# Kernel optimization log

Measured on AMD Instinct MI355X. Metric: run time of the kernel, lower is better.

## Reference

```python
import jax, jax.numpy as jnp
import numpy as np

B, S, D, H, FF = 2, 4096, 1024, 16, 4096
HD = D // H


def _layernorm(x, g, b, eps=1e-5):
    mu = jnp.mean(x, axis=-1, keepdims=True)
    var = jnp.var(x, axis=-1, keepdims=True)
    return (x - mu) * jax.lax.rsqrt(var + eps) * g + b


def setup_inputs() -> dict:
    key = jax.random.key(0)
    ks = jax.random.split(key, 20)
    sd = 1.0 / np.sqrt(D)
    sf = 1.0 / np.sqrt(FF)
    inp = {
        "x": jax.random.normal(ks[0], (B, S, D), jnp.float32),
        # attention projections, stored as [in, out]
        "wq": jax.random.normal(ks[1], (D, D), jnp.float32) * sd,
        "bq": jnp.zeros((D,), jnp.float32),
        "wk": jax.random.normal(ks[2], (D, D), jnp.float32) * sd,
        "bk": jnp.zeros((D,), jnp.float32),
        "wv": jax.random.normal(ks[3], (D, D), jnp.float32) * sd,
        "bv": jnp.zeros((D,), jnp.float32),
        "wo": jax.random.normal(ks[4], (D, D), jnp.float32) * sd,
        "bo": jnp.zeros((D,), jnp.float32),
        # block norm1 (pre-attention)
        "ln1_g": jnp.ones((D,), jnp.float32),
        "ln1_b": jnp.zeros((D,), jnp.float32),
        # FFN internal norm
        "lnf_g": jnp.ones((D,), jnp.float32),
        "lnf_b": jnp.zeros((D,), jnp.float32),
        # gated FFN
        "w1": jax.random.normal(ks[5], (D, FF), jnp.float32) * sd,
        "b1": jnp.zeros((FF,), jnp.float32),
        "wg": jax.random.normal(ks[6], (D, FF), jnp.float32) * sd,
        "bg": jnp.zeros((FF,), jnp.float32),
        "w2": jax.random.normal(ks[7], (FF, D), jnp.float32) * sf,
        "b2": jnp.zeros((D,), jnp.float32),
    }
    return inp


def reference(x, wq, bq, wk, bk, wv, bv, wo, bo, ln1_g, ln1_b,
              lnf_g, lnf_b, w1, b1, wg, bg, w2, b2):
    # pre-norm attention
    residual = x
    h = _layernorm(x, ln1_g, ln1_b)
    q = (h @ wq + bq).reshape(B, S, H, HD).transpose(0, 2, 1, 3)  # [B,H,S,hd]
    k = (h @ wk + bk).reshape(B, S, H, HD).transpose(0, 2, 1, 3)
    v = (h @ wv + bv).reshape(B, S, H, HD).transpose(0, 2, 1, 3)
    scores = jnp.einsum("bhqd,bhkd->bhqk", q, k) / np.sqrt(HD)
    attn = jax.nn.softmax(scores, axis=-1)  # [B,H,S,S] materialized as in torch src
    ctx = jnp.einsum("bhqk,bhkd->bhqd", attn, v)
    ctx = ctx.transpose(0, 2, 1, 3).reshape(B, S, D)
    attn_out = ctx @ wo + bo
    x = residual + attn_out  # dropout = 0 (eval)

    # gated FFN with internal pre-norm and residual
    res2 = x
    h2 = _layernorm(x, lnf_g, lnf_b)
    gate = jax.nn.sigmoid(h2 @ wg + bg)
    up = jax.nn.gelu(h2 @ w1 + b1, approximate=False)
    out = (up * gate) @ w2 + b2
    return out + res2
```

## Files before the change

kernel.cpp:

```cpp
#include <hip/hip_runtime.h>
#include <hip/hip_bf16.h>

#define BB 2
#define SS 4096
#define DD 1024
#define HH 16
#define HD 64
#define FF 4096
#define MM (BB*SS)

typedef __hip_bfloat16 bf16;
typedef __attribute__((ext_vector_type(8))) __bf16 v8bf;
typedef __attribute__((ext_vector_type(4))) float f32x4;
typedef __attribute__((ext_vector_type(16))) float f32x16;
typedef __attribute__((ext_vector_type(8))) unsigned short u16v8;

__device__ __forceinline__ f32x4 mfma16(v8bf a, v8bf b, f32x4 c) {
  return __builtin_amdgcn_mfma_f32_16x16x32_bf16(a, b, c, 0, 0, 0);
}
__device__ __forceinline__ f32x16 mfma32(v8bf a, v8bf b, f32x16 c) {
  return __builtin_amdgcn_mfma_f32_32x32x16_bf16(a, b, c, 0, 0, 0);
}
__device__ __forceinline__ void gload16(const void* g, void* l) {
  __builtin_amdgcn_global_load_lds((const __attribute__((address_space(1))) void*)g,
                                   (__attribute__((address_space(3))) void*)l, 16, 0, 0);
}
__device__ __forceinline__ unsigned cvtpk_bf16(float lo, float hi) {
  unsigned r;
  asm("v_cvt_pk_bf16_f32 %0, %1, %2" : "=v"(r) : "v"(lo), "v"(hi));
  return r;
}
__device__ __forceinline__ void xcd_swz(int& bx, int& by) {
  const int nwg = gridDim.x * gridDim.y;
  int o = blockIdx.y * gridDim.x + blockIdx.x;
  o = (o & 7) * (nwg >> 3) + (o >> 3);
  bx = o % gridDim.x;
  by = o / gridDim.x;
}

__global__ void k_tcvt(const float* __restrict__ W, bf16* __restrict__ Wt, int K, int N,
                       float scale)
{
  __shared__ float tile[32][33];
  const int n0 = blockIdx.x * 32, k0 = blockIdx.y * 32;
  const int tx = threadIdx.x, ty = threadIdx.y;
#pragma unroll
  for (int i = 0; i < 32; i += 8)
    tile[ty + i][tx] = W[(long)(k0 + ty + i) * N + n0 + tx];
  __syncthreads();
#pragma unroll
  for (int i = 0; i < 32; i += 8)
    Wt[(long)(n0 + ty + i) * K + k0 + tx] = __float2bfloat16(tile[tx][ty + i] * scale);
}

__global__ __launch_bounds__(256)
void k_vtrans(const bf16* __restrict__ V, bf16* __restrict__ Vt)
{
  __shared__ bf16 tile[64][72];
  const int s0 = blockIdx.x * 64;
  const int h  = blockIdx.y;
  const int b  = blockIdx.z;
  const int t  = threadIdx.x;
  const int r = t >> 3, c8 = t & 7;
#pragma unroll
  for (int it = 0; it < 2; ++it) {
    const int sr = it * 32 + r;
    const u16v8 v = *(const u16v8*)(V + (long)(b * SS + s0 + sr) * DD + h * 64 + c8 * 8);
#pragma unroll
    for (int e = 0; e < 8; ++e)
      ((unsigned short*)&tile[sr][0])[c8 * 8 + e] = v[e];
  }
  __syncthreads();
#pragma unroll
  for (int it = 0; it < 2; ++it) {
    const int d = it * 32 + r;
    union { unsigned short s[8]; u16v8 v; } o;
#pragma unroll
    for (int e = 0; e < 8; ++e)
      o.s[e] = ((const unsigned short*)tile)[(c8 * 8 + e) * 72 + d];
    *(u16v8*)(Vt + ((long)(b * HH + h) * HD + d) * (long)SS + s0 + c8 * 8) = o.v;
  }
}

__global__ __launch_bounds__(256)
void k_layernorm(const float* __restrict__ x, const float* __restrict__ g,
                 const float* __restrict__ b, bf16* __restrict__ out)
{
  const int row = blockIdx.x;
  const float4 v = ((const float4*)(x + (long)row * DD))[threadIdx.x];
  float s  = v.x + v.y + v.z + v.w;
  float s2 = v.x*v.x + v.y*v.y + v.z*v.z + v.w*v.w;
#pragma unroll
  for (int off = 1; off < 64; off <<= 1) {
    s  += __shfl_xor(s,  off);
    s2 += __shfl_xor(s2, off);
  }
  __shared__ float red[8];
  if ((threadIdx.x & 63) == 0) {
    red[threadIdx.x >> 6]       = s;
    red[(threadIdx.x >> 6) + 4] = s2;
  }
  __syncthreads();
  s  = red[0] + red[1] + red[2] + red[3];
  s2 = red[4] + red[5] + red[6] + red[7];
  const float mu = s * (1.f / DD);
  const float rs = rsqrtf(s2 * (1.f / DD) - mu * mu + 1e-5f);
  const float4 gv = ((const float4*)g)[threadIdx.x];
  const float4 bv = ((const float4*)b)[threadIdx.x];
  bf16* op = out + (long)row * DD + threadIdx.x * 4;
  op[0] = __float2bfloat16((v.x - mu) * rs * gv.x + bv.x);
  op[1] = __float2bfloat16((v.y - mu) * rs * gv.y + bv.y);
  op[2] = __float2bfloat16((v.z - mu) * rs * gv.z + bv.z);
  op[3] = __float2bfloat16((v.w - mu) * rs * gv.w + bv.w);
}

template<int EPI, int SWZ>
__global__ __launch_bounds__(256, 2)
void k_gemm(const bf16* __restrict__ A, const bf16* __restrict__ Bt,
            const float* __restrict__ bias, const float* __restrict__ res,
            void* __restrict__ Cout, int M, int N, int K, float scale)
{
  __shared__ __align__(16) bf16 As[128 * 32];
  __shared__ __align__(16) bf16 Bs[128 * 32];
  int bx = blockIdx.x, by = blockIdx.y;
  if (SWZ) xcd_swz(bx, by);
  const int t = threadIdx.x;
  const int lane = t & 63, w = t >> 6;
  const int wr = w >> 1, wc = w & 1;
  const int fr = lane & 15, fq = lane >> 4;
  const long m0 = (long)by * 128, n0 = (long)bx * 128;

  f32x4 acc[4][4] = {};

  const bf16* Ag0 = A  + (m0 + (t >> 2)) * K + (t & 3) * 8;
  const bf16* Ag1 = Ag0 + 64L * K;
  const bf16* Bg0 = Bt + (n0 + (t >> 2)) * K + (t & 3) * 8;
  const bf16* Bg1 = Bg0 + 64L * K;

  for (int kk = 0; kk < K; kk += 32) {
    gload16(Ag0 + kk, As + t * 8);
    gload16(Ag1 + kk, As + 2048 + t * 8);
    gload16(Bg0 + kk, Bs + t * 8);
    gload16(Bg1 + kk, Bs + 2048 + t * 8);
    __syncthreads();
    v8bf af[4], bfr[4];
#pragma unroll
    for (int mt = 0; mt < 4; ++mt)
      af[mt] = *(const v8bf*)&As[(wr*64 + mt*16 + fr) * 32 + fq*8];
#pragma unroll
    for (int nt = 0; nt < 4; ++nt)
      bfr[nt] = *(const v8bf*)&Bs[(wc*64 + nt*16 + fr) * 32 + fq*8];
#pragma unroll
    for (int mt = 0; mt < 4; ++mt)
#pragma unroll
      for (int nt = 0; nt < 4; ++nt)
        acc[mt][nt] = mfma16(af[mt], bfr[nt], acc[mt][nt]);
    __syncthreads();
  }

#pragma unroll
  for (int nt = 0; nt < 4; ++nt) {
    const long col = n0 + wc*64 + nt*16 + fr;
    const float bv = bias[col];
#pragma unroll
    for (int mt = 0; mt < 4; ++mt) {
#pragma unroll
      for (int j = 0; j < 4; ++j) {
        const long row = m0 + wr*64 + mt*16 + fq*4 + j;
        float v = (acc[mt][nt][j] + bv) * scale;
        if (EPI == 0) ((bf16*)Cout)[row * N + col] = __float2bfloat16(v);
        else          ((float*)Cout)[row * N + col] = v + res[row * N + col];
      }
    }
  }
}

__global__ __launch_bounds__(256, 2)
void k_ffn_dual(const bf16* __restrict__ A, const bf16* __restrict__ BgT,
                const bf16* __restrict__ BuT, const float* __restrict__ bgb,
                const float* __restrict__ bub, bf16* __restrict__ Out)
{
  __shared__ __align__(16) bf16 As[128 * 32];
  __shared__ __align__(16) bf16 Gs[64 * 32];
  __shared__ __align__(16) bf16 Us[64 * 32];
  const int t = threadIdx.x;
  const int lane = t & 63, w = t >> 6;
  const int wr = w >> 1, wc = w & 1;
  const int fr = lane & 15, fq = lane >> 4;
  const long m0 = (long)blockIdx.y * 128, n0 = (long)blockIdx.x * 64;
  const int K = DD;

  f32x4 ag[4][2] = {}, au[4][2] = {};

  const bf16* Ag0 = A   + (m0 + (t >> 2)) * K + (t & 3) * 8;
  const bf16* Ag1 = Ag0 + 64L * K;
  const bf16* Gg  = BgT + (n0 + (t >> 2)) * K + (t & 3) * 8;
  const bf16* Ug  = BuT + (n0 + (t >> 2)) * K + (t & 3) * 8;

  for (int kk = 0; kk < K; kk += 32) {
    gload16(Ag0 + kk, As + t * 8);
    gload16(Ag1 + kk, As + 2048 + t * 8);
    gload16(Gg + kk, Gs + t * 8);
    gload16(Ug + kk, Us + t * 8);
    __syncthreads();
    v8bf af[4], gf[2], uf[2];
#pragma unroll
    for (int mt = 0; mt < 4; ++mt)
      af[mt] = *(const v8bf*)&As[(wr*64 + mt*16 + fr) * 32 + fq*8];
#pragma unroll
    for (int nt = 0; nt < 2; ++nt) {
      gf[nt] = *(const v8bf*)&Gs[(wc*32 + nt*16 + fr) * 32 + fq*8];
      uf[nt] = *(const v8bf*)&Us[(wc*32 + nt*16 + fr) * 32 + fq*8];
    }
#pragma unroll
    for (int mt = 0; mt < 4; ++mt)
#pragma unroll
      for (int nt = 0; nt < 2; ++nt) {
        ag[mt][nt] = mfma16(af[mt], gf[nt], ag[mt][nt]);
        au[mt][nt] = mfma16(af[mt], uf[nt], au[mt][nt]);
      }
    __syncthreads();
  }

#pragma unroll
  for (int nt = 0; nt < 2; ++nt) {
    const long col = n0 + wc*32 + nt*16 + fr;
    const float gb = bgb[col], ub = bub[col];
#pragma unroll
    for (int mt = 0; mt < 4; ++mt) {
#pragma unroll
      for (int j = 0; j < 4; ++j) {
        const long row = m0 + wr*64 + mt*16 + fq*4 + j;
        const float g = ag[mt][nt][j] + gb;
        const float u = au[mt][nt][j] + ub;
        const float sg = 1.f / (1.f + __expf(-g));
        const float gl = 0.5f * u * (1.f + erff(u * 0.70710678118f));
        Out[row * FF + col] = __float2bfloat16(sg * gl);
      }
    }
  }
}

__global__ __launch_bounds__(256, 2)
void k_attn(const bf16* __restrict__ Qb, const bf16* __restrict__ Kb,
            const bf16* __restrict__ Vt, bf16* __restrict__ ctx)
{
  __shared__ __align__(16) bf16 Ksh[2][4096];
  __shared__ __align__(16) bf16 Vsh[2][4096];
  const int t = threadIdx.x;
  const int lane = t & 63, w = t >> 6;
  const int q5 = lane & 31, hi = lane >> 5;

  int o = blockIdx.x + 32 * (blockIdx.y + 16 * blockIdx.z);
  o = (o & 7) * 128 + (o >> 3);
  const int q0 = (o & 31) * 128;
  const int h = (o >> 5) & 15, b = o >> 9;

  const long qk_base = ((long)b * SS) * DD + h * HD;
  const long vt_base = ((long)(b * HH + h)) * ((long)HD * SS);

  const int r0 = t >> 3;
  const int cswz = ((t & 7) * 16) ^ ((r0 & 7) << 4);
  const bf16* kg = Kb + qk_base + (long)r0 * DD + (cswz >> 1);
  const bf16* vg = Vt + vt_base + (long)r0 * SS + (cswz >> 1);

  v8bf qf[4];
  {
    const bf16* qp = Qb + qk_base + (long)(q0 + w * 32 + q5) * DD + hi * 8;
#pragma unroll
    for (int c = 0; c < 4; ++c) qf[c] = *(const v8bf*)(qp + c * 16);
  }

  int kcol[4];
#pragma unroll
  for (int c = 0; c < 4; ++c)
    kcol[c] = ((c * 32 + hi * 16) ^ ((q5 & 7) << 4)) >> 1;

  float m_ = -1e30f, l_ = 0.f;
  f32x16 o0 = {}, o1 = {};

#define STAGE(bufidx, kv0_) do {                                  \
    const bf16* kp_ = kg + (long)(kv0_) * DD;                     \
    gload16(kp_,            &Ksh[bufidx][t * 8]);                 \
    gload16(kp_ + 32L * DD, &Ksh[bufidx][2048 + t * 8]);          \
    const bf16* vp_ = vg + (kv0_);                                \
    gload16(vp_,            &Vsh[bufidx][t * 8]);                 \
    gload16(vp_ + 32L * SS, &Vsh[bufidx][2048 + t * 8]);          \
  } while (0)

  STAGE(0, 0);
  __syncthreads();

  for (int tt = 0; tt < SS / 64; ++tt) {
    const int cur = tt & 1;
    if (tt + 1 < SS / 64) STAGE(cur ^ 1, (tt + 1) * 64);

    f32x16 s0 = {}, s1 = {};
#pragma unroll
    for (int c = 0; c < 4; ++c) {
      const v8bf k0 = *(const v8bf*)&Ksh[cur][q5 * 64 + kcol[c]];
      const v8bf k1 = *(const v8bf*)&Ksh[cur][(32 + q5) * 64 + kcol[c]];
      s0 = mfma32(k0, qf[c], s0);
      s1 = mfma32(k1, qf[c], s1);
    }

    float pm = s0[0];
#pragma unroll
    for (int r = 1; r < 16; ++r) pm = fmaxf(pm, s0[r]);
#pragma unroll
    for (int r = 0; r < 16; ++r) pm = fmaxf(pm, s1[r]);
    pm = fmaxf(pm, __shfl_xor(pm, 32));
    const float mn = fmaxf(m_, pm);
    const float al = __builtin_amdgcn_exp2f(m_ - mn);
    m_ = mn;
    float rs = 0.f;
#pragma unroll
    for (int r = 0; r < 16; ++r) { s0[r] = __builtin_amdgcn_exp2f(s0[r] - mn); rs += s0[r]; }
#pragma unroll
    for (int r = 0; r < 16; ++r) { s1[r] = __builtin_amdgcn_exp2f(s1[r] - mn); rs += s1[r]; }
    rs += __shfl_xor(rs, 32);
    l_ = l_ * al + rs;
#pragma unroll
    for (int r = 0; r < 16; ++r) { o0[r] *= al; o1[r] *= al; }

    v8bf pb[4];
#pragma unroll
    for (int c = 0; c < 4; ++c) {
      const int base = (c & 1) * 8;
      unsigned wa0, wa1, wb0, wb1;
      if (c < 2) {
        wa0 = cvtpk_bf16(s0[base + 0], s0[base + 1]);
        wa1 = cvtpk_bf16(s0[base + 2], s0[base + 3]);
        wb0 = cvtpk_bf16(s0[base + 4], s0[base + 5]);
        wb1 = cvtpk_bf16(s0[base + 6], s0[base + 7]);
      } else {
        wa0 = cvtpk_bf16(s1[base + 0], s1[base + 1]);
        wa1 = cvtpk_bf16(s1[base + 2], s1[base + 3]);
        wb0 = cvtpk_bf16(s1[base + 4], s1[base + 5]);
        wb1 = cvtpk_bf16(s1[base + 6], s1[base + 7]);
      }
      asm("v_permlane32_swap_b32 %0, %1" : "+v"(wa0), "+v"(wb0));
      asm("v_permlane32_swap_b32 %0, %1" : "+v"(wa1), "+v"(wb1));
      union { unsigned u[4]; v8bf v; } cvt;
      cvt.u[0] = wa0; cvt.u[1] = wa1; cvt.u[2] = wb0; cvt.u[3] = wb1;
      pb[c] = cvt.v;
    }

#pragma unroll
    for (int c = 0; c < 4; ++c) {
      const v8bf v0f = *(const v8bf*)&Vsh[cur][q5 * 64 + kcol[c]];
      const v8bf v1f = *(const v8bf*)&Vsh[cur][(32 + q5) * 64 + kcol[c]];
      o0 = mfma32(v0f, pb[c], o0);
      o1 = mfma32(v1f, pb[c], o1);
    }
    __syncthreads();
  }
#undef STAGE

  const float inv = 1.f / l_;
  bf16* Osh = &Ksh[0][0];
  const int qrow = w * 32 + q5;
  const int oswz = (qrow & 7) << 4;
#pragma unroll
  for (int r = 0; r < 16; ++r) {
    const int d0 = (r & 3) + 8 * (r >> 2) + 4 * hi;
    Osh[((qrow * 128 + d0 * 2) ^ oswz) >> 1]        = __float2bfloat16(o0[r] * inv);
    Osh[((qrow * 128 + (32 + d0) * 2) ^ oswz) >> 1] = __float2bfloat16(o1[r] * inv);
  }
  __syncthreads();
  {
    const int q = t >> 1, half = t & 1;
    const int qs = (q & 7) << 4;
    bf16* cp = ctx + qk_base + (long)(q0 + q) * DD + half * 32;
#pragma unroll
    for (int s = 0; s < 4; ++s) {
      const int byte = (q * 128 + half * 64 + s * 16) ^ qs;
      *(u16v8*)(cp + s * 8) = *(const u16v8*)&Osh[byte >> 1];
    }
  }
}

extern "C" void kernel_launch(void* const* d_in, const int* in_sizes, int n_in,
                              void* d_out, int out_size, void* d_ws, size_t ws_size,
                              hipStream_t stream)
{
  const float* x    = (const float*)d_in[0];
  const float* wq   = (const float*)d_in[1];
  const float* bq   = (const float*)d_in[2];
  const float* wk   = (const float*)d_in[3];
  const float* bk   = (const float*)d_in[4];
  const float* wv   = (const float*)d_in[5];
  const float* bv   = (const float*)d_in[6];
  const float* wo   = (const float*)d_in[7];
  const float* bo   = (const float*)d_in[8];
  const float* ln1g = (const float*)d_in[9];
  const float* ln1b = (const float*)d_in[10];
  const float* lnfg = (const float*)d_in[11];
  const float* lnfb = (const float*)d_in[12];
  const float* w1   = (const float*)d_in[13];
  const float* b1   = (const float*)d_in[14];
  const float* wg   = (const float*)d_in[15];
  const float* bg   = (const float*)d_in[16];
  const float* w2   = (const float*)d_in[17];
  const float* b2   = (const float*)d_in[18];

  char* ws = (char*)d_ws;
  const size_t MB = 1u << 20;
  bf16*  WqT  = (bf16*)(ws + 0 * MB);
  bf16*  WkT  = (bf16*)(ws + 2 * MB);
  bf16*  WvT  = (bf16*)(ws + 4 * MB);
  bf16*  WoT  = (bf16*)(ws + 6 * MB);
  bf16*  W1T  = (bf16*)(ws + 8 * MB);
  bf16*  WgT  = (bf16*)(ws + 16 * MB);
  bf16*  W2T  = (bf16*)(ws + 24 * MB);
  float* x1   = (float*)(ws + 32 * MB);
  bf16*  hbuf = (bf16*)(ws + 64 * MB);
  bf16*  Qb   = (bf16*)(ws + 80 * MB);
  bf16*  Kb   = (bf16*)(ws + 96 * MB);
  bf16*  Vb   = (bf16*)(ws + 112 * MB);
  bf16*  Vtb  = (bf16*)(ws + 128 * MB);
  bf16*  ctxb = hbuf;
  bf16*  prod = (bf16*)(ws + 80 * MB);

  const float qscale = 0.1803368801111204f;

  dim3 tb(32, 8);
  k_tcvt<<<dim3(32, 32), tb, 0, stream>>>(wq, WqT, 1024, 1024, 1.f);
  k_tcvt<<<dim3(32, 32), tb, 0, stream>>>(wk, WkT, 1024, 1024, 1.f);
  k_tcvt<<<dim3(32, 32), tb, 0, stream>>>(wv, WvT, 1024, 1024, 1.f);
  k_tcvt<<<dim3(32, 32), tb, 0, stream>>>(wo, WoT, 1024, 1024, 1.f);
  k_tcvt<<<dim3(128, 32), tb, 0, stream>>>(w1, W1T, 1024, 4096, 1.f);
  k_tcvt<<<dim3(128, 32), tb, 0, stream>>>(wg, WgT, 1024, 4096, 1.f);
  k_tcvt<<<dim3(32, 128), tb, 0, stream>>>(w2, W2T, 4096, 1024, 1.f);

  k_layernorm<<<MM, 256, 0, stream>>>(x, ln1g, ln1b, hbuf);

  dim3 g1(1024 / 128, MM / 128);
  k_gemm<0,1><<<g1, 256, 0, stream>>>(hbuf, WqT, bq, nullptr, Qb, MM, 1024, 1024, qscale);
  k_gemm<0,1><<<g1, 256, 0, stream>>>(hbuf, WkT, bk, nullptr, Kb, MM, 1024, 1024, 1.f);
  k_gemm<0,1><<<g1, 256, 0, stream>>>(hbuf, WvT, bv, nullptr, Vb, MM, 1024, 1024, 1.f);
  k_vtrans<<<dim3(SS / 64, HH, BB), 256, 0, stream>>>(Vb, Vtb);

  k_attn<<<dim3(SS / 128, HH, BB), 256, 0, stream>>>(Qb, Kb, Vtb, ctxb);

  k_gemm<1,1><<<g1, 256, 0, stream>>>(ctxb, WoT, bo, x, x1, MM, 1024, 1024, 1.f);

  k_layernorm<<<MM, 256, 0, stream>>>(x1, lnfg, lnfb, hbuf);

  k_ffn_dual<<<dim3(FF / 64, MM / 128), 256, 0, stream>>>(hbuf, WgT, W1T, bg, b1, prod);

  k_gemm<1,0><<<g1, 256, 0, stream>>>(prod, W2T, b2, x1, (float*)d_out, MM, 1024, 4096, 1.f);
}
```

Measured before the change: 621.3 us.

## Fuse QKV GEMMs, approximate GELU/sigmoid, add lazy softmax rescaling, drop swizzle

Concatenates Wq/Wk/Wv into one transposed weight, with the Q scale folded into the weights, and runs a single 3072-wide GEMM whose epilogue selects the bias per segment. The attention and V-transpose kernels read directly from the fused QKV buffer. The FFN epilogue replaces erf-GELU with a tanh-style exp approximation and uses hardware rcp for the sigmoid. Attention skips the online-softmax rescale when the running max grows by at most 8, and the XCD swizzle is disabled for every GEMM. These changes aim to cut launch overhead, redundant A-tile loads, and transcendental cost, at the price of some accuracy and possibly worse L2 locality.

After: 619.7 us. No clear change (-0.3%).

```diff
diff --git a/kernel.cpp b/kernel.cpp
--- a/kernel.cpp
+++ b/kernel.cpp
@@ -8,6 +8,7 @@
 #define HD 64
 #define FF 4096
 #define MM (BB*SS)
+#define QKVW 3072
 
 typedef __hip_bfloat16 bf16;
 typedef __attribute__((ext_vector_type(8))) __bf16 v8bf;
@@ -30,16 +31,14 @@
   asm("v_cvt_pk_bf16_f32 %0, %1, %2" : "=v"(r) : "v"(lo), "v"(hi));
   return r;
 }
-__device__ __forceinline__ void xcd_swz(int& bx, int& by) {
-  const int nwg = gridDim.x * gridDim.y;
-  int o = blockIdx.y * gridDim.x + blockIdx.x;
-  o = (o & 7) * (nwg >> 3) + (o >> 3);
-  bx = o % gridDim.x;
-  by = o / gridDim.x;
+__device__ __forceinline__ float fastrcp(float x) {
+  float r;
+  asm("v_rcp_f32 %0, %1" : "=v"(r) : "v"(x));
+  return r;
 }
 
 __global__ void k_tcvt(const float* __restrict__ W, bf16* __restrict__ Wt, int K, int N,
-                       float scale)
+                       long rowoff, float scale)
 {
   __shared__ float tile[32][33];
   const int n0 = blockIdx.x * 32, k0 = blockIdx.y * 32;
@@ -50,11 +49,11 @@
   __syncthreads();
 #pragma unroll
   for (int i = 0; i < 32; i += 8)
-    Wt[(long)(n0 + ty + i) * K + k0 + tx] = __float2bfloat16(tile[tx][ty + i] * scale);
+    Wt[(rowoff + n0 + ty + i) * K + k0 + tx] = __float2bfloat16(tile[tx][ty + i] * scale);
 }
 
 __global__ __launch_bounds__(256)
-void k_vtrans(const bf16* __restrict__ V, bf16* __restrict__ Vt)
+void k_vtrans(const bf16* __restrict__ qkv, bf16* __restrict__ Vt)
 {
   __shared__ bf16 tile[64][72];
   const int s0 = blockIdx.x * 64;
@@ -65,7 +64,8 @@
 #pragma unroll
   for (int it = 0; it < 2; ++it) {
     const int sr = it * 32 + r;
-    const u16v8 v = *(const u16v8*)(V + (long)(b * SS + s0 + sr) * DD + h * 64 + c8 * 8);
+    const u16v8 v =
+        *(const u16v8*)(qkv + (long)(b * SS + s0 + sr) * QKVW + 2048 + h * 64 + c8 * 8);
 #pragma unroll
     for (int e = 0; e < 8; ++e)
       ((unsigned short*)&tile[sr][0])[c8 * 8 + e] = v[e];
@@ -117,13 +117,20 @@
 template<int EPI, int SWZ>
 __global__ __launch_bounds__(256, 2)
 void k_gemm(const bf16* __restrict__ A, const bf16* __restrict__ Bt,
-            const float* __restrict__ bias, const float* __restrict__ res,
+            const float* __restrict__ bias, const float* __restrict__ bias2,
+            const float* __restrict__ bias3, const float* __restrict__ res,
             void* __restrict__ Cout, int M, int N, int K, float scale)
 {
   __shared__ __align__(16) bf16 As[128 * 32];
   __shared__ __align__(16) bf16 Bs[128 * 32];
   int bx = blockIdx.x, by = blockIdx.y;
-  if (SWZ) xcd_swz(bx, by);
+  if (SWZ) {
+    const int nwg = gridDim.x * gridDim.y;
+    int o = by * gridDim.x + bx;
+    o = (o & 7) * (nwg >> 3) + (o >> 3);
+    bx = o % gridDim.x;
+    by = o / gridDim.x;
+  }
   const int t = threadIdx.x;
   const int lane = t & 63, w = t >> 6;
   const int wr = w >> 1, wc = w & 1;
@@ -161,14 +168,21 @@
 #pragma unroll
   for (int nt = 0; nt < 4; ++nt) {
     const long col = n0 + wc*64 + nt*16 + fr;
-    const float bv = bias[col];
+    float bv;
+    if (EPI == 2) {
+      const int seg = (int)(col >> 10);
+      bv = (seg == 0) ? bias[col & 1023] * scale
+                      : ((seg == 1) ? bias2 : bias3)[col & 1023];
+    } else {
+      bv = bias[col];
+    }
 #pragma unroll
     for (int mt = 0; mt < 4; ++mt) {
 #pragma unroll
       for (int j = 0; j < 4; ++j) {
         const long row = m0 + wr*64 + mt*16 + fq*4 + j;
-        float v = (acc[mt][nt][j] + bv) * scale;
-        if (EPI == 0) ((bf16*)Cout)[row * N + col] = __float2bfloat16(v);
+        const float v = acc[mt][nt][j] + bv;
+        if (EPI == 2) ((bf16*)Cout)[row * N + col] = __float2bfloat16(v);
         else          ((float*)Cout)[row * N + col] = v + res[row * N + col];
       }
     }
@@ -233,8 +247,11 @@
         const long row = m0 + wr*64 + mt*16 + fq*4 + j;
         const float g = ag[mt][nt][j] + gb;
         const float u = au[mt][nt][j] + ub;
-        const float sg = 1.f / (1.f + __expf(-g));
-        const float gl = 0.5f * u * (1.f + erff(u * 0.70710678118f));
+        const float eg = __builtin_amdgcn_exp2f(1.44269504f * g);
+        const float sg = eg * fastrcp(1.f + eg);
+        const float u3 = u * u * u;
+        const float E = __builtin_amdgcn_exp2f(fmaf(0.1029453f, u3, 2.3021858f * u));
+        const float gl = u * E * fastrcp(1.f + E);
         Out[row * FF + col] = __float2bfloat16(sg * gl);
       }
     }
@@ -242,8 +259,8 @@
 }
 
 __global__ __launch_bounds__(256, 2)
-void k_attn(const bf16* __restrict__ Qb, const bf16* __restrict__ Kb,
-            const bf16* __restrict__ Vt, bf16* __restrict__ ctx)
+void k_attn(const bf16* __restrict__ qkv, const bf16* __restrict__ Vt,
+            bf16* __restrict__ ctx)
 {
   __shared__ __align__(16) bf16 Ksh[2][4096];
   __shared__ __align__(16) bf16 Vsh[2][4096];
@@ -256,17 +273,18 @@
   const int q0 = (o & 31) * 128;
   const int h = (o >> 5) & 15, b = o >> 9;
 
-  const long qk_base = ((long)b * SS) * DD + h * HD;
-  const long vt_base = ((long)(b * HH + h)) * ((long)HD * SS);
+  const long qkv_row0 = (long)b * SS * QKVW + h * HD;
+  const long ctx_base = (long)b * SS * DD + h * HD;
+  const long vt_base  = ((long)(b * HH + h)) * ((long)HD * SS);
 
   const int r0 = t >> 3;
   const int cswz = ((t & 7) * 16) ^ ((r0 & 7) << 4);
-  const bf16* kg = Kb + qk_base + (long)r0 * DD + (cswz >> 1);
+  const bf16* kg = qkv + qkv_row0 + 1024 + (long)r0 * QKVW + (cswz >> 1);
   const bf16* vg = Vt + vt_base + (long)r0 * SS + (cswz >> 1);
 
   v8bf qf[4];
   {
-    const bf16* qp = Qb + qk_base + (long)(q0 + w * 32 + q5) * DD + hi * 8;
+    const bf16* qp = qkv + qkv_row0 + (long)(q0 + w * 32 + q5) * QKVW + hi * 8;
 #pragma unroll
     for (int c = 0; c < 4; ++c) qf[c] = *(const v8bf*)(qp + c * 16);
   }
@@ -279,13 +297,13 @@
   float m_ = -1e30f, l_ = 0.f;
   f32x16 o0 = {}, o1 = {};
 
-#define STAGE(bufidx, kv0_) do {                                  \
-    const bf16* kp_ = kg + (long)(kv0_) * DD;                     \
-    gload16(kp_,            &Ksh[bufidx][t * 8]);                 \
-    gload16(kp_ + 32L * DD, &Ksh[bufidx][2048 + t * 8]);          \
-    const bf16* vp_ = vg + (kv0_);                                \
-    gload16(vp_,            &Vsh[bufidx][t * 8]);                 \
-    gload16(vp_ + 32L * SS, &Vsh[bufidx][2048 + t * 8]);          \
+#define STAGE(bufidx, kv0_) do {                                    \
+    const bf16* kp_ = kg + (long)(kv0_) * QKVW;                     \
+    gload16(kp_,              &Ksh[bufidx][t * 8]);                 \
+    gload16(kp_ + 32L * QKVW, &Ksh[bufidx][2048 + t * 8]);          \
+    const bf16* vp_ = vg + (kv0_);                                  \
+    gload16(vp_,            &Vsh[bufidx][t * 8]);                   \
+    gload16(vp_ + 32L * SS, &Vsh[bufidx][2048 + t * 8]);            \
   } while (0)
 
   STAGE(0, 0);
@@ -310,18 +328,28 @@
 #pragma unroll
     for (int r = 0; r < 16; ++r) pm = fmaxf(pm, s1[r]);
     pm = fmaxf(pm, __shfl_xor(pm, 32));
-    const float mn = fmaxf(m_, pm);
-    const float al = __builtin_amdgcn_exp2f(m_ - mn);
-    m_ = mn;
+
     float rs = 0.f;
-#pragma unroll
-    for (int r = 0; r < 16; ++r) { s0[r] = __builtin_amdgcn_exp2f(s0[r] - mn); rs += s0[r]; }
-#pragma unroll
-    for (int r = 0; r < 16; ++r) { s1[r] = __builtin_amdgcn_exp2f(s1[r] - mn); rs += s1[r]; }
-    rs += __shfl_xor(rs, 32);
-    l_ = l_ * al + rs;
-#pragma unroll
-    for (int r = 0; r < 16; ++r) { o0[r] *= al; o1[r] *= al; }
+    if (__all(pm - m_ <= 8.f)) {
+#pragma unroll
+      for (int r = 0; r < 16; ++r) { s0[r] = __builtin_amdgcn_exp2f(s0[r] - m_); rs += s0[r]; }
+#pragma unroll
+      for (int r = 0; r < 16; ++r) { s1[r] = __builtin_amdgcn_exp2f(s1[r] - m_); rs += s1[r]; }
+      rs += __shfl_xor(rs, 32);
+      l_ += rs;
+    } else {
+      const float mn = fmaxf(m_, pm);
+      const float al = __builtin_amdgcn_exp2f(m_ - mn);
+      m_ = mn;
+#pragma unroll
+      for (int r = 0; r < 16; ++r) { s0[r] = __builtin_amdgcn_exp2f(s0[r] - mn); rs += s0[r]; }
+#pragma unroll
+      for (int r = 0; r < 16; ++r) { s1[r] = __builtin_amdgcn_exp2f(s1[r] - mn); rs += s1[r]; }
+      rs += __shfl_xor(rs, 32);
+      l_ = l_ * al + rs;
+#pragma unroll
+      for (int r = 0; r < 16; ++r) { o0[r] *= al; o1[r] *= al; }
+    }
 
     v8bf pb[4];
 #pragma unroll
@@ -371,7 +399,7 @@
   {
     const int q = t >> 1, half = t & 1;
     const int qs = (q & 7) << 4;
-    bf16* cp = ctx + qk_base + (long)(q0 + q) * DD + half * 32;
+    bf16* cp = ctx + ctx_base + (long)(q0 + q) * DD + half * 32;
 #pragma unroll
     for (int s = 0; s < 4; ++s) {
       const int byte = (q * 128 + half * 64 + s * 16) ^ qs;
@@ -406,48 +434,44 @@
 
   char* ws = (char*)d_ws;
   const size_t MB = 1u << 20;
-  bf16*  WqT  = (bf16*)(ws + 0 * MB);
-  bf16*  WkT  = (bf16*)(ws + 2 * MB);
-  bf16*  WvT  = (bf16*)(ws + 4 * MB);
-  bf16*  WoT  = (bf16*)(ws + 6 * MB);
-  bf16*  W1T  = (bf16*)(ws + 8 * MB);
-  bf16*  WgT  = (bf16*)(ws + 16 * MB);
-  bf16*  W2T  = (bf16*)(ws + 24 * MB);
-  float* x1   = (float*)(ws + 32 * MB);
-  bf16*  hbuf = (bf16*)(ws + 64 * MB);
-  bf16*  Qb   = (bf16*)(ws + 80 * MB);
-  bf16*  Kb   = (bf16*)(ws + 96 * MB);
-  bf16*  Vb   = (bf16*)(ws + 112 * MB);
-  bf16*  Vtb  = (bf16*)(ws + 128 * MB);
-  bf16*  ctxb = hbuf;
-  bf16*  prod = (bf16*)(ws + 80 * MB);
+  bf16*  WqkvT = (bf16*)(ws + 0 * MB);
+  bf16*  WoT   = (bf16*)(ws + 6 * MB);
+  bf16*  W1T   = (bf16*)(ws + 8 * MB);
+  bf16*  WgT   = (bf16*)(ws + 16 * MB);
+  bf16*  W2T   = (bf16*)(ws + 24 * MB);
+  float* x1    = (float*)(ws + 32 * MB);
+  bf16*  hbuf  = (bf16*)(ws + 64 * MB);
+  bf16*  QKVb  = (bf16*)(ws + 80 * MB);
+  bf16*  Vtb   = (bf16*)(ws + 128 * MB);
+  bf16*  ctxb  = hbuf;
+  bf16*  prod  = (bf16*)(ws + 80 * MB);
 
   const float qscale = 0.1803368801111204f;
 
   dim3 tb(32, 8);
-  k_tcvt<<<dim3(32, 32), tb, 0, stream>>>(wq, WqT, 1024, 1024, 1.f);
-  k_tcvt<<<dim3(32, 32), tb, 0, stream>>>(wk, WkT, 1024, 1024, 1.f);
-  k_tcvt<<<dim3(32, 32), tb, 0, stream>>>(wv, WvT, 1024, 1024, 1.f);
-  k_tcvt<<<dim3(32, 32), tb, 0, stream>>>(wo, WoT, 1024, 1024, 1.f);
-  k_tcvt<<<dim3(128, 32), tb, 0, stream>>>(w1, W1T, 1024, 4096, 1.f);
-  k_tcvt<<<dim3(128, 32), tb, 0, stream>>>(wg, WgT, 1024, 4096, 1.f);
-  k_tcvt<<<dim3(32, 128), tb, 0, stream>>>(w2, W2T, 4096, 1024, 1.f);
+  k_tcvt<<<dim3(32, 32), tb, 0, stream>>>(wq, WqkvT, 1024, 1024, 0, qscale);
+  k_tcvt<<<dim3(32, 32), tb, 0, stream>>>(wk, WqkvT, 1024, 1024, 1024, 1.f);
+  k_tcvt<<<dim3(32, 32), tb, 0, stream>>>(wv, WqkvT, 1024, 1024, 2048, 1.f);
+  k_tcvt<<<dim3(32, 32), tb, 0, stream>>>(wo, WoT, 1024, 1024, 0, 1.f);
+  k_tcvt<<<dim3(128, 32), tb, 0, stream>>>(w1, W1T, 1024, 4096, 0, 1.f);
+  k_tcvt<<<dim3(128, 32), tb, 0, stream>>>(wg, WgT, 1024, 4096, 0, 1.f);
+  k_tcvt<<<dim3(32, 128), tb, 0, stream>>>(w2, W2T, 4096, 1024, 0, 1.f);
 
   k_layernorm<<<MM, 256, 0, stream>>>(x, ln1g, ln1b, hbuf);
 
-  dim3 g1(1024 / 128, MM / 128);
-  k_gemm<0,1><<<g1, 256, 0, stream>>>(hbuf, WqT, bq, nullptr, Qb, MM, 1024, 1024, qscale);
-  k_gemm<0,1><<<g1, 256, 0, stream>>>(hbuf, WkT, bk, nullptr, Kb, MM, 1024, 1024, 1.f);
-  k_gemm<0,1><<<g1, 256, 0, stream>>>(hbuf, WvT, bv, nullptr, Vb, MM, 1024, 1024, 1.f);
-  k_vtrans<<<dim3(SS / 64, HH, BB), 256, 0, stream>>>(Vb, Vtb);
-
-  k_attn<<<dim3(SS / 128, HH, BB), 256, 0, stream>>>(Qb, Kb, Vtb, ctxb);
-
-  k_gemm<1,1><<<g1, 256, 0, stream>>>(ctxb, WoT, bo, x, x1, MM, 1024, 1024, 1.f);
+  k_gemm<2,0><<<dim3(QKVW / 128, MM / 128), 256, 0, stream>>>(
+      hbuf, WqkvT, bq, bk, bv, nullptr, QKVb, MM, QKVW, 1024, qscale);
+
+  k_vtrans<<<dim3(SS / 64, HH, BB), 256, 0, stream>>>(QKVb, Vtb);
+  k_attn<<<dim3(SS / 128, HH, BB), 256, 0, stream>>>(QKVb, Vtb, ctxb);
+
+  k_gemm<1,0><<<dim3(8, 64), 256, 0, stream>>>(
+      ctxb, WoT, bo, nullptr, nullptr, x, x1, MM, 1024, 1024, 1.f);
 
   k_layernorm<<<MM, 256, 0, stream>>>(x1, lnfg, lnfb, hbuf);
 
   k_ffn_dual<<<dim3(FF / 64, MM / 128), 256, 0, stream>>>(hbuf, WgT, W1T, bg, b1, prod);
 
-  k_gemm<1,0><<<g1, 256, 0, stream>>>(prod, W2T, b2, x1, (float*)d_out, MM, 1024, 4096, 1.f);
-}
+  k_gemm<1,0><<<dim3(8, 64), 256, 0, stream>>>(
+      prod, W2T, b2, nullptr, nullptr, x1, (float*)d_out, MM, 1024, 4096, 1.f);
+}
```
